# Kernel tuning notes

Measured on AMD Instinct MI355X. Metric: run time of the kernel, lower is better.

## Reference

```python
import jax, jax.numpy as jnp
import numpy as np


def _conv1x1(x, W, b):
    # x: [B,C,H,W], W: [O,C], b: [O]  -> [B,O,H,W]
    return jnp.einsum('bchw,oc->bohw', x, W) + b[None, :, None, None]


def setup_inputs() -> dict:
    key = jax.random.key(0)
    ks = jax.random.split(key, 8)
    B, C, H, W = 16, 512, 48, 48
    d = C // 8
    scale = 0.02
    return {
        'feat_map': jax.random.normal(ks[0], (B, C, H, W), dtype=jnp.float32),
        'Wq': jax.random.normal(ks[1], (d, C), dtype=jnp.float32) * scale,
        'bq': jax.random.normal(ks[2], (d,), dtype=jnp.float32) * scale,
        'Wk': jax.random.normal(ks[3], (d, C), dtype=jnp.float32) * scale,
        'bk': jax.random.normal(ks[4], (d,), dtype=jnp.float32) * scale,
        'Wv': jax.random.normal(ks[5], (C, C), dtype=jnp.float32) * scale,
        'bv': jax.random.normal(ks[6], (C,), dtype=jnp.float32) * scale,
        'gamma': jnp.ones((1,), dtype=jnp.float32),
    }


def reference(feat_map, Wq, bq, Wk, bk, Wv, bv, gamma):
    # SAModule (DANet spatial attention):
    #   q = conv1(x) -> [B, d, HW] -> permute [B, HW, d]
    #   k = conv2(x) -> [B, d, HW]
    #   attn = softmax(q @ k, axis=-1)            # [B, HW, HW]
    #   v = conv3(x) -> [B, C, HW]
    #   out = v @ attn^T -> [B, C, H, W]
    #   y = gamma * out + x
    B, C, H, W = feat_map.shape
    HW = H * W
    q = _conv1x1(feat_map, Wq, bq).reshape(B, -1, HW).transpose(0, 2, 1)  # [B,HW,d]
    k = _conv1x1(feat_map, Wk, bk).reshape(B, -1, HW)                     # [B,d,HW]
    attn = jax.nn.softmax(jnp.einsum('bnd,bdm->bnm', q, k), axis=-1)      # [B,HW,HW]
    v = _conv1x1(feat_map, Wv, bv).reshape(B, C, HW)                      # [B,C,HW]
    out = jnp.einsum('bcm,bnm->bcn', v, attn).reshape(B, C, H, W)
    return gamma * out + feat_map
```

## Files before the change

kernel.cpp:

```cpp
#include <hip/hip_runtime.h>

typedef __bf16 bf16x8 __attribute__((ext_vector_type(8)));
typedef float  f32x4  __attribute__((ext_vector_type(4)));

constexpr int kHW = 2304;
constexpr int kC  = 512;

__device__ __forceinline__ void dma16(const __bf16* g, __bf16* l) {
    __builtin_amdgcn_global_load_lds(
        (const volatile __attribute__((address_space(1))) void*)g,
        (volatile __attribute__((address_space(3))) void*)l, 16, 0, 0);
}

__global__ void pack_weights(const float* __restrict__ Wq, const float* __restrict__ Wk,
                             const float* __restrict__ Wv, __bf16* __restrict__ Wqk2,
                             __bf16* __restrict__ Wvb2) {
    int idx = blockIdx.x * 256 + threadIdx.x;
    int o = idx >> 9, k = idx & 511, kb = k >> 6, kr = k & 63;
    if (idx < 64 * 512) {
        Wqk2[((size_t)kb * 128 + o) * 72 + kr]      = (__bf16)Wq[idx];
        Wqk2[((size_t)kb * 128 + 64 + o) * 72 + kr] = (__bf16)Wk[idx];
    }
    if (idx < 512 * 512)
        Wvb2[((size_t)kb * 512 + o) * 72 + kr] = (__bf16)Wv[idx];
}

__global__ void pack_x(const float* __restrict__ x, __bf16* __restrict__ XT2) {
    __shared__ __bf16 tile[64][65];
    int n0 = blockIdx.x * 64, kblk = blockIdx.y, b = blockIdx.z;
    int c0 = kblk * 64;
    int t = threadIdx.x;
    const float* xb = x + (size_t)b * kC * kHW;
#pragma unroll
    for (int rep = 0; rep < 16; ++rep) {
        int c_loc = rep * 4 + (t >> 6);
        int n_loc = t & 63;
        tile[c_loc][n_loc] = (__bf16)xb[(size_t)(c0 + c_loc) * kHW + n0 + n_loc];
    }
    __syncthreads();
    __bf16* dst = XT2 + ((size_t)b * 8 + kblk) * kHW * 72;
#pragma unroll
    for (int rep = 0; rep < 2; ++rep) {
        int item = rep * 256 + t;
        int n_loc = item >> 3, chunk = item & 7;
        bf16x8 v;
#pragma unroll
        for (int j = 0; j < 8; ++j) v[j] = tile[chunk * 8 + j][n_loc];
        *(bf16x8*)(dst + (size_t)(n0 + n_loc) * 72 + chunk * 8) = v;
    }
}

__global__ __launch_bounds__(256) void qkv_gemm(const __bf16* __restrict__ XT2,
                                                const __bf16* __restrict__ Wqk2,
                                                const __bf16* __restrict__ Wvb2,
                                                const float* __restrict__ bq,
                                                const float* __restrict__ bk,
                                                const float* __restrict__ bv,
                                                __bf16* __restrict__ qbuf,
                                                __bf16* __restrict__ kbuf,
                                                __bf16* __restrict__ vbuf2) {
    __shared__ __align__(16) __bf16 A_lds[128 * 72];
    __shared__ __align__(16) __bf16 B_lds[128 * 72];
    int r0 = blockIdx.x * 128, type = blockIdx.y, b = blockIdx.z;
    int t = threadIdx.x, wave = t >> 6, lane = t & 63, quad = lane >> 4, l16 = lane & 15;

    f32x4 acc[8][2];
#pragma unroll
    for (int i = 0; i < 8; ++i)
#pragma unroll
        for (int j = 0; j < 2; ++j) acc[i][j] = (f32x4){0.f, 0.f, 0.f, 0.f};

    for (int kb = 0; kb < 8; ++kb) {
        const __bf16* Asrc;
        const __bf16* Bsrc;
        if (type == 0) {
            Asrc = XT2 + (((size_t)b * 8 + kb) * kHW + r0) * 72;
            Bsrc = Wqk2 + (size_t)kb * 128 * 72;
        } else {
            Asrc = Wvb2 + ((size_t)kb * 512 + (type - 1) * 128) * 72;
            Bsrc = XT2 + (((size_t)b * 8 + kb) * kHW + r0) * 72;
        }
        __syncthreads();
        for (int ch = wave; ch < 18; ch += 4) {
            dma16(Asrc + ch * 512 + lane * 8, &A_lds[ch * 512]);
            dma16(Bsrc + ch * 512 + lane * 8, &B_lds[ch * 512]);
        }
        __syncthreads();
#pragma unroll
        for (int dk = 0; dk < 2; ++dk) {
            bf16x8 bfr[2];
#pragma unroll
            for (int ct = 0; ct < 2; ++ct)
                bfr[ct] = *(const bf16x8*)(&B_lds[(wave * 32 + ct * 16 + l16) * 72 + dk * 32 + quad * 8]);
#pragma unroll
            for (int rt = 0; rt < 8; ++rt) {
                bf16x8 a = *(const bf16x8*)(&A_lds[(rt * 16 + l16) * 72 + dk * 32 + quad * 8]);
#pragma unroll
                for (int ct = 0; ct < 2; ++ct)
                    acc[rt][ct] = __builtin_amdgcn_mfma_f32_16x16x32_bf16(a, bfr[ct], acc[rt][ct], 0, 0, 0);
            }
        }
    }

    if (type == 0) {
#pragma unroll
        for (int ct = 0; ct < 2; ++ct) {
            int o = wave * 32 + ct * 16 + l16;
            float bias = (o < 64) ? bq[o] : bk[o - 64];
#pragma unroll
            for (int rt = 0; rt < 8; ++rt)
#pragma unroll
                for (int r = 0; r < 4; ++r) {
                    int n = r0 + rt * 16 + quad * 4 + r;
                    __bf16 val = (__bf16)(acc[rt][ct][r] + bias);
                    if (o < 64)
                        qbuf[((size_t)b * kHW + n) * 64 + o] = val;
                    else
                        kbuf[(((size_t)b * 36 + (n >> 6)) * 64 + (n & 63)) * 72 + (o - 64)] = val;
                }
        }
    } else {
#pragma unroll
        for (int rt = 0; rt < 8; ++rt)
#pragma unroll
            for (int r = 0; r < 4; ++r) {
                int c = (type - 1) * 128 + rt * 16 + quad * 4 + r;
                float bias = bv[c];
#pragma unroll
                for (int ct = 0; ct < 2; ++ct) {
                    int m = r0 + wave * 32 + ct * 16 + l16;
                    vbuf2[(((size_t)b * 36 + (m >> 6)) * 512 + c) * 72 + (m & 63)] = (__bf16)(acc[rt][ct][r] + bias);
                }
            }
    }
}

__global__ __launch_bounds__(256, 2) void attn_kernel(const __bf16* __restrict__ qbuf,
                                                      const __bf16* __restrict__ kbuf,
                                                      const __bf16* __restrict__ vbuf2,
                                                      const float* __restrict__ x,
                                                      const float* __restrict__ gamma,
                                                      float* __restrict__ out) {
    __shared__ __align__(16) __bf16 K_lds[2][64 * 72];
    __shared__ __align__(16) __bf16 V_lds[2][128 * 72];
    __shared__ __align__(16) __bf16 P_lds[128 * 72];
    __shared__ float rs_lds[128];

    int n0 = blockIdx.x * 128, c0 = blockIdx.y * 128, b = blockIdx.z;
    int t = threadIdx.x, wave = t >> 6, lane = t & 63, quad = lane >> 4, l16 = lane & 15;
    const __bf16* q_b    = qbuf + (size_t)b * kHW * 64;
    const __bf16* k_base = kbuf + (size_t)b * 36 * 64 * 72;

    bf16x8 aq[2][2];
#pragma unroll
    for (int rt2 = 0; rt2 < 2; ++rt2)
#pragma unroll
        for (int dk = 0; dk < 2; ++dk)
            aq[rt2][dk] = *(const bf16x8*)(q_b + (size_t)(n0 + wave * 32 + rt2 * 16 + l16) * 64 + dk * 32 + quad * 8);

    f32x4 acc[8][2];
#pragma unroll
    for (int i = 0; i < 8; ++i)
#pragma unroll
        for (int j = 0; j < 2; ++j) acc[i][j] = (f32x4){0.f, 0.f, 0.f, 0.f};
    float rsum[2][4] = {{0.f, 0.f, 0.f, 0.f}, {0.f, 0.f, 0.f, 0.f}};

    auto issue_dma = [&](int i, int buf) {
        const __bf16* ks = k_base + (size_t)i * 64 * 72;
        const __bf16* vs = vbuf2 + (((size_t)b * 36 + i) * 512 + c0) * 72;
        for (int ch = wave; ch < 9; ch += 4)
            dma16(ks + ch * 512 + lane * 8, &K_lds[buf][ch * 512]);
        for (int ch = wave; ch < 18; ch += 4)
            dma16(vs + ch * 512 + lane * 8, &V_lds[buf][ch * 512]);
    };

    issue_dma(0, 0);
    for (int i = 0; i < 36; ++i) {
        int buf = i & 1;
        __syncthreads();
        if (i + 1 < 36) issue_dma(i + 1, buf ^ 1);
        bf16x8 vfrag[2][2];
#pragma unroll
        for (int ct = 0; ct < 2; ++ct)
#pragma unroll
            for (int dk = 0; dk < 2; ++dk)
                vfrag[ct][dk] = *(const bf16x8*)(&V_lds[buf][(wave * 32 + ct * 16 + l16) * 72 + dk * 32 + quad * 8]);
#pragma unroll
        for (int mt = 0; mt < 4; ++mt) {
            bf16x8 kf0 = *(const bf16x8*)(&K_lds[buf][(mt * 16 + l16) * 72 + quad * 8]);
            bf16x8 kf1 = *(const bf16x8*)(&K_lds[buf][(mt * 16 + l16) * 72 + 32 + quad * 8]);
#pragma unroll
            for (int rt2 = 0; rt2 < 2; ++rt2) {
                f32x4 s = (f32x4){0.f, 0.f, 0.f, 0.f};
                s = __builtin_amdgcn_mfma_f32_16x16x32_bf16(aq[rt2][0], kf0, s, 0, 0, 0);
                s = __builtin_amdgcn_mfma_f32_16x16x32_bf16(aq[rt2][1], kf1, s, 0, 0, 0);
#pragma unroll
                for (int r = 0; r < 4; ++r) {
                    __bf16 pb = (__bf16)__expf(s[r]);
                    rsum[rt2][r] += (float)pb;
                    P_lds[(wave * 32 + rt2 * 16 + quad * 4 + r) * 72 + mt * 16 + l16] = pb;
                }
            }
        }
        __syncthreads();
#pragma unroll
        for (int dk = 0; dk < 2; ++dk)
#pragma unroll
            for (int rt = 0; rt < 8; ++rt) {
                bf16x8 pf = *(const bf16x8*)(&P_lds[(rt * 16 + l16) * 72 + dk * 32 + quad * 8]);
                acc[rt][0] = __builtin_amdgcn_mfma_f32_16x16x32_bf16(pf, vfrag[0][dk], acc[rt][0], 0, 0, 0);
                acc[rt][1] = __builtin_amdgcn_mfma_f32_16x16x32_bf16(pf, vfrag[1][dk], acc[rt][1], 0, 0, 0);
            }
    }

#pragma unroll
    for (int rt2 = 0; rt2 < 2; ++rt2)
#pragma unroll
        for (int r = 0; r < 4; ++r) {
            float v = rsum[rt2][r];
            v += __shfl_xor(v, 1);
            v += __shfl_xor(v, 2);
            v += __shfl_xor(v, 4);
            v += __shfl_xor(v, 8);
            if (l16 == 0) rs_lds[wave * 32 + rt2 * 16 + quad * 4 + r] = v;
        }
    __syncthreads();

    float g = gamma[0];
    const float* x_b = x + (size_t)b * kC * kHW;
    float* out_b = out + (size_t)b * kC * kHW;
#pragma unroll
    for (int rt = 0; rt < 8; ++rt) {
        float inv[4];
#pragma unroll
        for (int r = 0; r < 4; ++r) inv[r] = 1.f / rs_lds[rt * 16 + quad * 4 + r];
#pragma unroll
        for (int ct = 0; ct < 2; ++ct) {
            int c = c0 + wave * 32 + ct * 16 + l16;
            size_t base = (size_t)c * kHW + n0 + rt * 16 + quad * 4;
            f32x4 xin = *(const f32x4*)(x_b + base);
            f32x4 y;
#pragma unroll
            for (int r = 0; r < 4; ++r) y[r] = g * acc[rt][ct][r] * inv[r] + xin[r];
            *(f32x4*)(out_b + base) = y;
        }
    }
}

extern "C" void kernel_launch(void* const* d_in, const int* in_sizes, int n_in,
                              void* d_out, int out_size, void* d_ws, size_t ws_size,
                              hipStream_t stream) {
    const float* x     = (const float*)d_in[0];
    const float* Wq    = (const float*)d_in[1];
    const float* bq    = (const float*)d_in[2];
    const float* Wk    = (const float*)d_in[3];
    const float* bk    = (const float*)d_in[4];
    const float* Wv    = (const float*)d_in[5];
    const float* bv    = (const float*)d_in[6];
    const float* gamma = (const float*)d_in[7];
    float* out = (float*)d_out;

    char* ws = (char*)d_ws;
    __bf16* XT2   = (__bf16*)(ws);
    __bf16* Wqk2  = (__bf16*)(ws + 42467328);
    __bf16* Wvb2  = (__bf16*)(ws + 42614784);
    __bf16* qbuf  = (__bf16*)(ws + 43204608);
    __bf16* kbuf  = (__bf16*)(ws + 47923200);
    __bf16* vbuf2 = (__bf16*)(ws + 53231616);

    hipLaunchKernelGGL(pack_weights, dim3(1024), dim3(256), 0, stream, Wq, Wk, Wv, Wqk2, Wvb2);
    hipLaunchKernelGGL(pack_x, dim3(36, 8, 16), dim3(256), 0, stream, x, XT2);
    hipLaunchKernelGGL(qkv_gemm, dim3(18, 5, 16), dim3(256), 0, stream,
                       XT2, Wqk2, Wvb2, bq, bk, bv, qbuf, kbuf, vbuf2);
    hipLaunchKernelGGL(attn_kernel, dim3(18, 4, 16), dim3(256), 0, stream,
                       qbuf, kbuf, vbuf2, x, gamma, out);
}
```

Baseline: 408.3 us.

## Make each wave own its P rows to drop mid-iteration barrier; use exp2

The attention kernel is reorganized so each wave computes and consumes only its own 32 query rows of P, with the S MFMA transposed so P is written as bf16x4 vectors. This removes the second __syncthreads per key tile; each wave now reads all 128 V columns from LDS instead of caching its own V fragments. Q is prescaled by log2(e) in the projection kernel so exp2 can replace expf. s_setprio is raised around the PV MFMA block. The trade is more LDS reads of V per wave in exchange for fewer barriers and cheaper exponentials.

```diff
diff --git a/kernel.cpp b/kernel.cpp
--- a/kernel.cpp
+++ b/kernel.cpp
@@ -1,10 +1,17 @@
 #include <hip/hip_runtime.h>
 
 typedef __bf16 bf16x8 __attribute__((ext_vector_type(8)));
+typedef __bf16 bf16x4 __attribute__((ext_vector_type(4)));
 typedef float  f32x4  __attribute__((ext_vector_type(4)));
 
 constexpr int kHW = 2304;
 constexpr int kC  = 512;
+
+#if __has_builtin(__builtin_amdgcn_exp2f)
+#define EXP2(x) __builtin_amdgcn_exp2f(x)
+#else
+#define EXP2(x) exp2f(x)
+#endif
 
 __device__ __forceinline__ void dma16(const __bf16* g, __bf16* l) {
     __builtin_amdgcn_global_load_lds(
@@ -103,16 +110,18 @@
     }
 
     if (type == 0) {
+        constexpr float kLog2e = 1.4426950408889634f;
 #pragma unroll
         for (int ct = 0; ct < 2; ++ct) {
             int o = wave * 32 + ct * 16 + l16;
             float bias = (o < 64) ? bq[o] : bk[o - 64];
+            float scale = (o < 64) ? kLog2e : 1.0f;
 #pragma unroll
             for (int rt = 0; rt < 8; ++rt)
 #pragma unroll
                 for (int r = 0; r < 4; ++r) {
                     int n = r0 + rt * 16 + quad * 4 + r;
-                    __bf16 val = (__bf16)(acc[rt][ct][r] + bias);
+                    __bf16 val = (__bf16)((acc[rt][ct][r] + bias) * scale);
                     if (o < 64)
                         qbuf[((size_t)b * kHW + n) * 64 + o] = val;
                     else
@@ -158,12 +167,12 @@
         for (int dk = 0; dk < 2; ++dk)
             aq[rt2][dk] = *(const bf16x8*)(q_b + (size_t)(n0 + wave * 32 + rt2 * 16 + l16) * 64 + dk * 32 + quad * 8);
 
-    f32x4 acc[8][2];
-#pragma unroll
-    for (int i = 0; i < 8; ++i)
-#pragma unroll
-        for (int j = 0; j < 2; ++j) acc[i][j] = (f32x4){0.f, 0.f, 0.f, 0.f};
-    float rsum[2][4] = {{0.f, 0.f, 0.f, 0.f}, {0.f, 0.f, 0.f, 0.f}};
+    f32x4 acc[2][8];
+#pragma unroll
+    for (int i = 0; i < 2; ++i)
+#pragma unroll
+        for (int j = 0; j < 8; ++j) acc[i][j] = (f32x4){0.f, 0.f, 0.f, 0.f};
+    float rsum[2] = {0.f, 0.f};
 
     auto issue_dma = [&](int i, int buf) {
         const __bf16* ks = k_base + (size_t)i * 64 * 72;
@@ -179,12 +188,8 @@
         int buf = i & 1;
         __syncthreads();
         if (i + 1 < 36) issue_dma(i + 1, buf ^ 1);
-        bf16x8 vfrag[2][2];
-#pragma unroll
-        for (int ct = 0; ct < 2; ++ct)
-#pragma unroll
-            for (int dk = 0; dk < 2; ++dk)
-                vfrag[ct][dk] = *(const bf16x8*)(&V_lds[buf][(wave * 32 + ct * 16 + l16) * 72 + dk * 32 + quad * 8]);
+
+        __bf16* prow = &P_lds[(wave * 32 + l16) * 72 + quad * 4];
 #pragma unroll
         for (int mt = 0; mt < 4; ++mt) {
             bf16x8 kf0 = *(const bf16x8*)(&K_lds[buf][(mt * 16 + l16) * 72 + quad * 8]);
@@ -192,56 +197,64 @@
 #pragma unroll
             for (int rt2 = 0; rt2 < 2; ++rt2) {
                 f32x4 s = (f32x4){0.f, 0.f, 0.f, 0.f};
-                s = __builtin_amdgcn_mfma_f32_16x16x32_bf16(aq[rt2][0], kf0, s, 0, 0, 0);
-                s = __builtin_amdgcn_mfma_f32_16x16x32_bf16(aq[rt2][1], kf1, s, 0, 0, 0);
+                s = __builtin_amdgcn_mfma_f32_16x16x32_bf16(kf0, aq[rt2][0], s, 0, 0, 0);
+                s = __builtin_amdgcn_mfma_f32_16x16x32_bf16(kf1, aq[rt2][1], s, 0, 0, 0);
+                bf16x4 pv;
+                float part = 0.f;
 #pragma unroll
                 for (int r = 0; r < 4; ++r) {
-                    __bf16 pb = (__bf16)__expf(s[r]);
-                    rsum[rt2][r] += (float)pb;
-                    P_lds[(wave * 32 + rt2 * 16 + quad * 4 + r) * 72 + mt * 16 + l16] = pb;
+                    pv[r] = (__bf16)EXP2(s[r]);
+                    part += (float)pv[r];
                 }
+                rsum[rt2] += part;
+                *(bf16x4*)(prow + rt2 * 16 * 72 + mt * 16) = pv;
             }
         }
-        __syncthreads();
-#pragma unroll
-        for (int dk = 0; dk < 2; ++dk)
-#pragma unroll
-            for (int rt = 0; rt < 8; ++rt) {
-                bf16x8 pf = *(const bf16x8*)(&P_lds[(rt * 16 + l16) * 72 + dk * 32 + quad * 8]);
-                acc[rt][0] = __builtin_amdgcn_mfma_f32_16x16x32_bf16(pf, vfrag[0][dk], acc[rt][0], 0, 0, 0);
-                acc[rt][1] = __builtin_amdgcn_mfma_f32_16x16x32_bf16(pf, vfrag[1][dk], acc[rt][1], 0, 0, 0);
-            }
-    }
-
-#pragma unroll
-    for (int rt2 = 0; rt2 < 2; ++rt2)
-#pragma unroll
-        for (int r = 0; r < 4; ++r) {
-            float v = rsum[rt2][r];
-            v += __shfl_xor(v, 1);
-            v += __shfl_xor(v, 2);
-            v += __shfl_xor(v, 4);
-            v += __shfl_xor(v, 8);
-            if (l16 == 0) rs_lds[wave * 32 + rt2 * 16 + quad * 4 + r] = v;
-        }
+
+        bf16x8 pf[2][2];
+#pragma unroll
+        for (int rt2 = 0; rt2 < 2; ++rt2)
+#pragma unroll
+            for (int dk = 0; dk < 2; ++dk)
+                pf[rt2][dk] = *(const bf16x8*)(&P_lds[(wave * 32 + rt2 * 16 + l16) * 72 + dk * 32 + quad * 8]);
+        __builtin_amdgcn_s_setprio(1);
+#pragma unroll
+        for (int ct = 0; ct < 8; ++ct) {
+            bf16x8 vf0 = *(const bf16x8*)(&V_lds[buf][(ct * 16 + l16) * 72 + quad * 8]);
+            bf16x8 vf1 = *(const bf16x8*)(&V_lds[buf][(ct * 16 + l16) * 72 + 32 + quad * 8]);
+            acc[0][ct] = __builtin_amdgcn_mfma_f32_16x16x32_bf16(pf[0][0], vf0, acc[0][ct], 0, 0, 0);
+            acc[0][ct] = __builtin_amdgcn_mfma_f32_16x16x32_bf16(pf[0][1], vf1, acc[0][ct], 0, 0, 0);
+            acc[1][ct] = __builtin_amdgcn_mfma_f32_16x16x32_bf16(pf[1][0], vf0, acc[1][ct], 0, 0, 0);
+            acc[1][ct] = __builtin_amdgcn_mfma_f32_16x16x32_bf16(pf[1][1], vf1, acc[1][ct], 0, 0, 0);
+        }
+        __builtin_amdgcn_s_setprio(0);
+    }
+
+#pragma unroll
+    for (int rt2 = 0; rt2 < 2; ++rt2) {
+        float v = rsum[rt2];
+        v += __shfl_xor(v, 16);
+        v += __shfl_xor(v, 32);
+        if (quad == 0) rs_lds[wave * 32 + rt2 * 16 + l16] = v;
+    }
     __syncthreads();
 
     float g = gamma[0];
     const float* x_b = x + (size_t)b * kC * kHW;
     float* out_b = out + (size_t)b * kC * kHW;
 #pragma unroll
-    for (int rt = 0; rt < 8; ++rt) {
+    for (int rt2 = 0; rt2 < 2; ++rt2) {
         float inv[4];
 #pragma unroll
-        for (int r = 0; r < 4; ++r) inv[r] = 1.f / rs_lds[rt * 16 + quad * 4 + r];
-#pragma unroll
-        for (int ct = 0; ct < 2; ++ct) {
-            int c = c0 + wave * 32 + ct * 16 + l16;
-            size_t base = (size_t)c * kHW + n0 + rt * 16 + quad * 4;
+        for (int r = 0; r < 4; ++r) inv[r] = 1.f / rs_lds[wave * 32 + rt2 * 16 + quad * 4 + r];
+#pragma unroll
+        for (int ct = 0; ct < 8; ++ct) {
+            int c = c0 + ct * 16 + l16;
+            size_t base = (size_t)c * kHW + n0 + wave * 32 + rt2 * 16 + quad * 4;
             f32x4 xin = *(const f32x4*)(x_b + base);
             f32x4 y;
 #pragma unroll
-            for (int r = 0; r < 4; ++r) y[r] = g * acc[rt][ct][r] * inv[r] + xin[r];
+            for (int r = 0; r < 4; ++r) y[r] = g * acc[rt2][ct][r] * inv[r] + xin[r];
             *(f32x4*)(out_b + base) = y;
         }
     }
```

Result: no change. 410.2 us (+0.5%).
